# Optimization experiments

Measured on AMD Instinct MI355X. Metric: run time of the kernel, lower is better.

Reference implementation:

```python
import jax, jax.numpy as jnp
import numpy as np

IN_DIM = 64
OUT_DIM = 64
N_MODES = 32


def setup_inputs() -> dict:
    key = jax.random.key(0)
    k_x, k_w0, k_w1 = jax.random.split(key, 3)
    x = jax.random.normal(k_x, (32, IN_DIM, 128, 128), dtype=jnp.float32)
    # xavier_normal_ on tensor of shape (in, out, modes, 2): fan_in = out*modes*2, fan_out = in*modes*2? 
    # torch treats dim0 as fan_out-ish; exact init scale is irrelevant for correctness baselines,
    # so use a matching gaussian std = sqrt(2/(in_dim+out_dim)).
    std = float(np.sqrt(2.0 / (IN_DIM + OUT_DIM)))
    w0 = std * jax.random.normal(k_w0, (IN_DIM, OUT_DIM, N_MODES, 2), dtype=jnp.float32)
    w1 = std * jax.random.normal(k_w1, (IN_DIM, OUT_DIM, N_MODES, 2), dtype=jnp.float32)
    return {"x": x, "w0": w0, "w1": w1}


def reference(x, w0, w1):
    B, I, M, N = x.shape
    n_modes = w0.shape[2]

    # ---- width (last-axis) branch ----
    x_fty = jnp.fft.rfft(x, axis=-1, norm='ortho')                      # [B, I, M, N//2+1]
    wc0 = w0[..., 0] + 1j * w0[..., 1]                                  # [I, O, n_modes]
    low_y = jnp.einsum('bixy,ioy->boxy', x_fty[..., :n_modes], wc0)     # [B, O, M, n_modes]
    out_ft_y = jnp.pad(low_y, ((0, 0), (0, 0), (0, 0), (0, N // 2 + 1 - n_modes)))
    xy = jnp.fft.irfft(out_ft_y, n=N, axis=-1, norm='ortho')            # [B, O, M, N]

    # ---- height (second-to-last axis) branch ----
    x_ftx = jnp.fft.rfft(x, axis=-2, norm='ortho')                      # [B, I, M//2+1, N]
    wc1 = w1[..., 0] + 1j * w1[..., 1]                                  # [I, O, n_modes]
    low_x = jnp.einsum('bixy,iox->boxy', x_ftx[:, :, :n_modes, :], wc1)  # [B, O, n_modes, N]
    out_ft_x = jnp.pad(low_x, ((0, 0), (0, 0), (0, M // 2 + 1 - n_modes), (0, 0)))
    xx = jnp.fft.irfft(out_ft_x, n=M, axis=-2, norm='ortho')            # [B, O, M, N]

    return xx + xy
```

## Files before the change

### kernel.cpp

```cpp
#include <hip/hip_runtime.h>


typedef _Float16 half8  __attribute__((ext_vector_type(8)));
typedef _Float16 half4v __attribute__((ext_vector_type(4)));
typedef _Float16 half2v __attribute__((ext_vector_type(2)));
typedef float    floatx4 __attribute__((ext_vector_type(4)));

#define TWO_PI_OVER_128 0.049087385212340517f

__device__ __forceinline__ unsigned int packh2(float a, float b) {
    half2v h; h[0] = (_Float16)a; h[1] = (_Float16)b;
    return __builtin_bit_cast(unsigned int, h);
}
__device__ __forceinline__ half8  ash8(uint4 u) { return __builtin_bit_cast(half8, u); }
__device__ __forceinline__ half4v ash4(uint2 u) { return __builtin_bit_cast(half4v, u); }

#define MFMA_K16(A,B,C) __builtin_amdgcn_mfma_f32_16x16x16f16((A),(B),(C),0,0,0)

#define YS_PK 324
#define YS_PR 20

__global__ __launch_bounds__(256) void w2expand(const float* __restrict__ w0,
                                                const float* __restrict__ w1,
                                                uint2* __restrict__ W2h)
{
    int g = blockIdx.x * 256 + threadIdx.x;
    const float* w = (g >> 17) ? w1 : w0;
    int e    = g & 131071;
    int lane = e & 63;
    int m    = (e >> 6) & 7;
    int c    = (e >> 9) & 7;
    int k    = e >> 12;
    int mrow = lane & 15, q = lane >> 4;
    int o  = (m * 16 + mrow) >> 1;
    int oc = mrow & 1;
    unsigned int h2[2];
#pragma unroll
    for (int hp = 0; hp < 2; ++hp) {
        int i = c * 8 + q * 2 + hp;
        const float* wp = w + ((i * 64 + o) * 32 + k) * 2;
        float re = wp[0], im = wp[1];
        float v0 = oc ? im : re;
        float v1 = oc ? re : -im;
        h2[hp] = packh2(v0, v1);
    }
    W2h[g] = make_uint2(h2[0], h2[1]);
}

template<int BR>
__global__ __launch_bounds__(512, 4) void spectral(const float* __restrict__ x,
                                                   const uint2* __restrict__ w2,
                                                   float* __restrict__ out)
{
    __shared__ uint4 Ubuf[34816 / 16];
    __shared__ unsigned short Ys[32 * YS_PK];

    unsigned short* Xs = (unsigned short*)Ubuf;
    unsigned int*   Zs = (unsigned int*)Ubuf;

    const int tid  = threadIdx.x;
    const int wv   = tid >> 6;
    const int lane = tid & 63;
    const int mrow = tid & 15;
    const int quad = (tid >> 4) & 3;
    const int bx   = blockIdx.x;
    const int oh   = bx & 1;
    const int tile = (bx >> 1) & 7;
    const int b    = bx >> 4;

    const long xb = (long)b * 1048576 + (BR == 0 ? tile * 2048 : tile * 16);
    const long ob = xb;

    const int kptile = wv & 3;
    half8 Ff[4];
#pragma unroll
    for (int s = 0; s < 4; ++s)
#pragma unroll
        for (int j = 0; j < 8; ++j) {
            int d  = s * 32 + quad * 8 + j;
            int kp = kptile * 16 + mrow;
            int k  = kp >> 1;
            float ang = TWO_PI_OVER_128 * (float)((k * d) & 127);
            float v = (kp & 1) ? -sinf(ang) : cosf(ang);
            Ff[s][j] = (_Float16)v;
        }

    floatx4 acc[2][2][4];
#pragma unroll
    for (int a = 0; a < 2; ++a)
#pragma unroll
        for (int kk = 0; kk < 2; ++kk)
#pragma unroll
            for (int m = 0; m < 4; ++m)
                acc[a][kk][m] = (floatx4){0.f, 0.f, 0.f, 0.f};


#pragma unroll
    for (int g = 0; g < 2; ++g) {
        float4 v[4];
#pragma unroll
        for (int pp = 0; pp < 4; ++pp) {
            int p = g * 4 + pp;
            if (BR == 0) {
                int idx = p * 512 + tid;
                int col = idx >> 5, dg = idx & 31;
                v[pp] = *(const float4*)(x + xb + (long)(col >> 4) * 16384 + (col & 15) * 128 + dg * 4);
            } else {
                int d = (tid >> 2) & 127, tq = (tid & 3) * 4;
                v[pp] = *(const float4*)(x + xb + (long)p * 16384 + d * 128 + tq);
            }
        }
#pragma unroll
        for (int pp = 0; pp < 4; ++pp) {
            int p = g * 4 + pp;
            if (BR == 0) {
                int idx = p * 512 + tid;
                int col = idx >> 5, dg = idx & 31;
                *(uint2*)&Xs[col * 136 + dg * 4] =
                    make_uint2(packh2(v[pp].x, v[pp].y), packh2(v[pp].z, v[pp].w));
            } else {
                int d = (tid >> 2) & 127, tq = (tid & 3) * 4;
                int colb = p * 16 + tq;
                Xs[(colb + 0) * 136 + d] = __builtin_bit_cast(unsigned short, (_Float16)v[pp].x);
                Xs[(colb + 1) * 136 + d] = __builtin_bit_cast(unsigned short, (_Float16)v[pp].y);
                Xs[(colb + 2) * 136 + d] = __builtin_bit_cast(unsigned short, (_Float16)v[pp].z);
                Xs[(colb + 3) * 136 + d] = __builtin_bit_cast(unsigned short, (_Float16)v[pp].w);
            }
        }
    }
    __syncthreads();

    for (int c = 0; c < 8; ++c) {
        float4 pfA[4];
        if (c < 7) {
#pragma unroll
            for (int p = 0; p < 4; ++p) {
                if (BR == 0) {
                    int idx = p * 512 + tid;
                    int col = idx >> 5, dg = idx & 31;
                    pfA[p] = *(const float4*)(x + xb + (long)((c + 1) * 8 + (col >> 4)) * 16384 + (col & 15) * 128 + dg * 4);
                } else {
                    int d = (tid >> 2) & 127, tq = (tid & 3) * 4;
                    pfA[p] = *(const float4*)(x + xb + (long)((c + 1) * 8 + p) * 16384 + d * 128 + tq);
                }
            }
        }

#pragma unroll
        for (int cc = 0; cc < 4; ++cc) {
            int i = (wv >> 2) * 4 + cc;
            floatx4 y4 = {0.f, 0.f, 0.f, 0.f};
#pragma unroll
            for (int s = 0; s < 4; ++s) {
                uint4 bv = *(const uint4*)&Xs[(i * 16 + mrow) * 136 + s * 32 + quad * 8];
                y4 = __builtin_amdgcn_mfma_f32_16x16x32_f16(Ff[s], ash8(bv), y4, 0, 0, 0);
            }
            int k0 = kptile * 8 + quad * 2;
            unsigned int* yw = (unsigned int*)Ys;
            yw[(k0    ) * (YS_PK / 2) + mrow * (YS_PR / 2) + i] = packh2(y4[0], y4[1]);
            yw[(k0 + 1) * (YS_PK / 2) + mrow * (YS_PR / 2) + i] = packh2(y4[2], y4[3]);
        }
        __syncthreads();

        float4 pfB[4];
        if (c < 7) {
#pragma unroll
            for (int p = 0; p < 4; ++p) {
                if (BR == 0) {
                    int idx = p * 512 + tid;
                    int col = idx >> 5, dg = idx & 31;
                    *(uint2*)&Xs[col * 136 + dg * 4] =
                        make_uint2(packh2(pfA[p].x, pfA[p].y), packh2(pfA[p].z, pfA[p].w));
                } else {
                    int d = (tid >> 2) & 127, tq = (tid & 3) * 4;
                    int colb = p * 16 + tq;
                    Xs[(colb + 0) * 136 + d] = __builtin_bit_cast(unsigned short, (_Float16)pfA[p].x);
                    Xs[(colb + 1) * 136 + d] = __builtin_bit_cast(unsigned short, (_Float16)pfA[p].y);
                    Xs[(colb + 2) * 136 + d] = __builtin_bit_cast(unsigned short, (_Float16)pfA[p].z);
                    Xs[(colb + 3) * 136 + d] = __builtin_bit_cast(unsigned short, (_Float16)pfA[p].w);
                }
            }
#pragma unroll
            for (int p = 0; p < 4; ++p) {
                if (BR == 0) {
                    int idx = (p + 4) * 512 + tid;
                    int col = idx >> 5, dg = idx & 31;
                    pfB[p] = *(const float4*)(x + xb + (long)((c + 1) * 8 + (col >> 4)) * 16384 + (col & 15) * 128 + dg * 4);
                } else {
                    int d = (tid >> 2) & 127, tq = (tid & 3) * 4;
                    pfB[p] = *(const float4*)(x + xb + (long)((c + 1) * 8 + 4 + p) * 16384 + d * 128 + tq);
                }
            }
        }

        {
            half4v bfA0 = ash4(*(const uint2*)&Ys[(2 * wv     ) * YS_PK + mrow * YS_PR + quad * 4]);
            half4v bfA1 = ash4(*(const uint2*)&Ys[(2 * wv + 1 ) * YS_PK + mrow * YS_PR + quad * 4]);
            half4v bfB0 = ash4(*(const uint2*)&Ys[(2 * wv + 16) * YS_PK + mrow * YS_PR + quad * 4]);
            half4v bfB1 = ash4(*(const uint2*)&Ys[(2 * wv + 17) * YS_PK + mrow * YS_PR + quad * 4]);
            const uint2* wpA = w2 + (((2 * wv) * 8 + c) * 8 + oh * 4) * 64 + lane;
            const uint2* wpB = wpA + 65536;
#pragma unroll
            for (int m = 0; m < 4; ++m) {
                acc[0][0][m] = MFMA_K16(ash4(wpA[m * 64       ]), bfA0, acc[0][0][m]);
                acc[0][1][m] = MFMA_K16(ash4(wpA[m * 64 + 4096]), bfA1, acc[0][1][m]);
                acc[1][0][m] = MFMA_K16(ash4(wpB[m * 64       ]), bfB0, acc[1][0][m]);
                acc[1][1][m] = MFMA_K16(ash4(wpB[m * 64 + 4096]), bfB1, acc[1][1][m]);
            }
        }

        if (c < 7) {
#pragma unroll
            for (int p = 0; p < 4; ++p) {
                if (BR == 0) {
                    int idx = (p + 4) * 512 + tid;
                    int col = idx >> 5, dg = idx & 31;
                    *(uint2*)&Xs[col * 136 + dg * 4] =
                        make_uint2(packh2(pfB[p].x, pfB[p].y), packh2(pfB[p].z, pfB[p].w));
                } else {
                    int d = (tid >> 2) & 127, tq = (tid & 3) * 4;
                    int colb = (4 + p) * 16 + tq;
                    Xs[(colb + 0) * 136 + d] = __builtin_bit_cast(unsigned short, (_Float16)pfB[p].x);
                    Xs[(colb + 1) * 136 + d] = __builtin_bit_cast(unsigned short, (_Float16)pfB[p].y);
                    Xs[(colb + 2) * 136 + d] = __builtin_bit_cast(unsigned short, (_Float16)pfB[p].z);
                    Xs[(colb + 3) * 136 + d] = __builtin_bit_cast(unsigned short, (_Float16)pfB[p].w);
                }
            }
        }
        __syncthreads();
    }

    const int dt = wv;
    const int dp = dt * 16 + mrow;
    half8 Gf[2];
#pragma unroll
    for (int s = 0; s < 2; ++s)
#pragma unroll
        for (int j = 0; j < 8; ++j) {
            int kp = s * 32 + quad * 8 + j;
            int k  = kp >> 1;
            float ang = TWO_PI_OVER_128 * (float)((k * dp) & 127);
            float v;
            if (kp == 0)      v = 1.f / 128.f;
            else if (kp == 1) v = 0.f;
            else v = (kp & 1) ? -(2.f / 128.f) * sinf(ang) : (2.f / 128.f) * cosf(ang);
            Gf[s][j] = (_Float16)v;
        }

#pragma unroll
    for (int q = 0; q < 4; ++q) {
        __syncthreads();
#pragma unroll
        for (int a = 0; a < 2; ++a)
#pragma unroll
            for (int kk = 0; kk < 2; ++kk) {
                const int kmode = 2 * (wv + a * 8) + kk;
                const int slot  = kmode ^ (quad * 8);
                const int col   = (quad * 2) * 16 + mrow;
                Zs[ col       * 36 + slot] = packh2(acc[a][kk][q][0], acc[a][kk][q][1]);
                Zs[(col + 16) * 36 + slot] = packh2(acc[a][kk][q][2], acc[a][kk][q][3]);
            }
        __syncthreads();

#pragma unroll
        for (int cc = 0; cc < 8; ++cc) {
            const int ct  = cc;
            const int col = ct * 16 + mrow;
            const int swz = (ct & 6) << 2;
            floatx4 o4 = {0.f, 0.f, 0.f, 0.f};
#pragma unroll
            for (int s = 0; s < 2; ++s) {
                uint4 zv = *(const uint4*)&Zs[col * 36 + ((s * 16 + quad * 4) ^ swz)];
                o4 = __builtin_amdgcn_mfma_f32_16x16x32_f16(Gf[s], ash8(zv), o4, 0, 0, 0);
            }
            const int oo = oh * 32 + q * 8 + ct;
            const int t  = mrow;
            const int db = dt * 16 + quad * 4;
            if (BR == 0) {
                __builtin_nontemporal_store(o4, (floatx4*)(out + ob + (long)oo * 16384 + t * 128 + db));
            } else {
                float* p = out + ob + (long)oo * 16384 + (long)db * 128 + t;
                unsafeAtomicAdd(p,       o4[0]);
                unsafeAtomicAdd(p + 128, o4[1]);
                unsafeAtomicAdd(p + 256, o4[2]);
                unsafeAtomicAdd(p + 384, o4[3]);
            }
        }
    }
}

extern "C" void kernel_launch(void* const* d_in, const int* in_sizes, int n_in,
                              void* d_out, int out_size, void* d_ws, size_t ws_size,
                              hipStream_t stream) {
    const float* x  = (const float*)d_in[0];
    const float* w0 = (const float*)d_in[1];
    const float* w1 = (const float*)d_in[2];
    float* out = (float*)d_out;

    uint2* W2h = (uint2*)d_ws;

    w2expand<<<dim3(1024), dim3(256), 0, stream>>>(w0, w1, W2h);

    dim3 grid(512);
    dim3 block(512);

    spectral<0><<<grid, block, 0, stream>>>(x, W2h,          out);
    spectral<1><<<grid, block, 0, stream>>>(x, W2h + 131072, out);
}
```

Measured before the change: 574.5 us.

## Merge output-channel halves into one 1024-thread block with K32 MFMA mixing

Each block now covers all 64 output channels for its tile with 1024 threads, instead of two blocks each handling half the outputs and both redoing the forward DFT of the same input tile. The channel-mixing step switches from 16x16x16 to 16x16x32 MFMAs over 16 input channels per chunk, and the weight-expansion kernel writes a matching uint4 layout. This removes the duplicated input loads and forward DFT work. In exchange the grid drops to 256 blocks, and each block uses twice the shared memory and carries larger accumulator register tiles, which may lower occupancy.

```diff
diff --git a/kernel.cpp b/kernel.cpp
--- a/kernel.cpp
+++ b/kernel.cpp
@@ -2,7 +2,6 @@
 
 
 typedef _Float16 half8  __attribute__((ext_vector_type(8)));
-typedef _Float16 half4v __attribute__((ext_vector_type(4)));
 typedef _Float16 half2v __attribute__((ext_vector_type(2)));
 typedef float    floatx4 __attribute__((ext_vector_type(4)));
 
@@ -12,47 +11,51 @@
     half2v h; h[0] = (_Float16)a; h[1] = (_Float16)b;
     return __builtin_bit_cast(unsigned int, h);
 }
-__device__ __forceinline__ half8  ash8(uint4 u) { return __builtin_bit_cast(half8, u); }
-__device__ __forceinline__ half4v ash4(uint2 u) { return __builtin_bit_cast(half4v, u); }
-
-#define MFMA_K16(A,B,C) __builtin_amdgcn_mfma_f32_16x16x16f16((A),(B),(C),0,0,0)
-
-#define YS_PK 324
-#define YS_PR 20
+__device__ __forceinline__ half8 ash8(uint4 u) { return __builtin_bit_cast(half8, u); }
+
+#define MFMA_K32(A,B,C) __builtin_amdgcn_mfma_f32_16x16x32_f16((A),(B),(C),0,0,0)
+
+#define YS_PR 40
+#define YS_PK 648
 
 __global__ __launch_bounds__(256) void w2expand(const float* __restrict__ w0,
                                                 const float* __restrict__ w1,
-                                                uint2* __restrict__ W2h)
+                                                uint4* __restrict__ W2h)
 {
     int g = blockIdx.x * 256 + threadIdx.x;
-    const float* w = (g >> 17) ? w1 : w0;
-    int e    = g & 131071;
+    const float* w = (g >> 16) ? w1 : w0;
+    int e    = g & 65535;
     int lane = e & 63;
     int m    = (e >> 6) & 7;
-    int c    = (e >> 9) & 7;
-    int k    = e >> 12;
-    int mrow = lane & 15, q = lane >> 4;
+    int c4   = (e >> 9) & 3;
+    int k    = e >> 11;
+    int mrow = lane & 15, quad = lane >> 4;
     int o  = (m * 16 + mrow) >> 1;
     int oc = mrow & 1;
-    unsigned int h2[2];
-#pragma unroll
-    for (int hp = 0; hp < 2; ++hp) {
-        int i = c * 8 + q * 2 + hp;
-        const float* wp = w + ((i * 64 + o) * 32 + k) * 2;
-        float re = wp[0], im = wp[1];
-        float v0 = oc ? im : re;
-        float v1 = oc ? re : -im;
-        h2[hp] = packh2(v0, v1);
+    unsigned int hw[4];
+#pragma unroll
+    for (int jp = 0; jp < 4; ++jp) {
+        float v[2];
+#pragma unroll
+        for (int jj = 0; jj < 2; ++jj) {
+            int r    = quad * 8 + jp * 2 + jj;
+            int i    = c4 * 16 + (r >> 1);
+            int comp = r & 1;
+            const float* wp = w + ((i * 64 + o) * 32 + k) * 2;
+            float re = wp[0], im = wp[1];
+            v[jj] = oc ? (comp ? re : im) : (comp ? -im : re);
+        }
+        hw[jp] = packh2(v[0], v[1]);
     }
-    W2h[g] = make_uint2(h2[0], h2[1]);
+    W2h[g] = make_uint4(hw[0], hw[1], hw[2], hw[3]);
 }
 
 template<int BR>
-__global__ __launch_bounds__(512, 4) void spectral(const float* __restrict__ x,
-                                                   const uint2* __restrict__ w2,
-                                                   float* __restrict__ out)
+__global__ __launch_bounds__(1024, 4) void spectral(const float* __restrict__ x,
+                                                    const uint4* __restrict__ w2,
+                                                    float* __restrict__ out)
 {
-    __shared__ uint4 Ubuf[34816 / 16];
+    __shared__ uint4 Ubuf[69632 / 16];
     __shared__ unsigned short Ys[32 * YS_PK];
 
     unsigned short* Xs = (unsigned short*)Ubuf;
@@ -64,14 +67,14 @@
     const int mrow = tid & 15;
     const int quad = (tid >> 4) & 3;
     const int bx   = blockIdx.x;
-    const int oh   = bx & 1;
-    const int tile = (bx >> 1) & 7;
-    const int b    = bx >> 4;
+    const int b    = bx >> 3;
+    const int tile = bx & 7;
 
     const long xb = (long)b * 1048576 + (BR == 0 ? tile * 2048 : tile * 16);
     const long ob = xb;
 
     const int kptile = wv & 3;
+    const int igrp   = wv >> 2;
     half8 Ff[4];
 #pragma unroll
     for (int s = 0; s < 4; ++s)
@@ -85,15 +88,12 @@
             Ff[s][j] = (_Float16)v;
         }
 
-    floatx4 acc[2][2][4];
-#pragma unroll
-    for (int a = 0; a < 2; ++a)
-#pragma unroll
-        for (int kk = 0; kk < 2; ++kk)
-#pragma unroll
-            for (int m = 0; m < 4; ++m)
-                acc[a][kk][m] = (floatx4){0.f, 0.f, 0.f, 0.f};
-
+    floatx4 acc[2][8];
+#pragma unroll
+    for (int kk = 0; kk < 2; ++kk)
+#pragma unroll
+        for (int m = 0; m < 8; ++m)
+            acc[kk][m] = (floatx4){0.f, 0.f, 0.f, 0.f};
 
 #pragma unroll
     for (int g = 0; g < 2; ++g) {
@@ -102,25 +102,27 @@
         for (int pp = 0; pp < 4; ++pp) {
             int p = g * 4 + pp;
             if (BR == 0) {
-                int idx = p * 512 + tid;
+                int idx = p * 1024 + tid;
                 int col = idx >> 5, dg = idx & 31;
                 v[pp] = *(const float4*)(x + xb + (long)(col >> 4) * 16384 + (col & 15) * 128 + dg * 4);
             } else {
+                int i = (tid >> 9) + p * 2;
                 int d = (tid >> 2) & 127, tq = (tid & 3) * 4;
-                v[pp] = *(const float4*)(x + xb + (long)p * 16384 + d * 128 + tq);
+                v[pp] = *(const float4*)(x + xb + (long)i * 16384 + d * 128 + tq);
             }
         }
 #pragma unroll
         for (int pp = 0; pp < 4; ++pp) {
             int p = g * 4 + pp;
             if (BR == 0) {
-                int idx = p * 512 + tid;
+                int idx = p * 1024 + tid;
                 int col = idx >> 5, dg = idx & 31;
                 *(uint2*)&Xs[col * 136 + dg * 4] =
                     make_uint2(packh2(v[pp].x, v[pp].y), packh2(v[pp].z, v[pp].w));
             } else {
+                int i = (tid >> 9) + p * 2;
                 int d = (tid >> 2) & 127, tq = (tid & 3) * 4;
-                int colb = p * 16 + tq;
+                int colb = i * 16 + tq;
                 Xs[(colb + 0) * 136 + d] = __builtin_bit_cast(unsigned short, (_Float16)v[pp].x);
                 Xs[(colb + 1) * 136 + d] = __builtin_bit_cast(unsigned short, (_Float16)v[pp].y);
                 Xs[(colb + 2) * 136 + d] = __builtin_bit_cast(unsigned short, (_Float16)v[pp].z);
@@ -130,25 +132,26 @@
     }
     __syncthreads();
 
-    for (int c = 0; c < 8; ++c) {
+    for (int c = 0; c < 4; ++c) {
         float4 pfA[4];
-        if (c < 7) {
+        if (c < 3) {
 #pragma unroll
             for (int p = 0; p < 4; ++p) {
                 if (BR == 0) {
-                    int idx = p * 512 + tid;
+                    int idx = p * 1024 + tid;
                     int col = idx >> 5, dg = idx & 31;
-                    pfA[p] = *(const float4*)(x + xb + (long)((c + 1) * 8 + (col >> 4)) * 16384 + (col & 15) * 128 + dg * 4);
+                    pfA[p] = *(const float4*)(x + xb + (long)((c + 1) * 16 + (col >> 4)) * 16384 + (col & 15) * 128 + dg * 4);
                 } else {
+                    int i = (tid >> 9) + p * 2;
                     int d = (tid >> 2) & 127, tq = (tid & 3) * 4;
-                    pfA[p] = *(const float4*)(x + xb + (long)((c + 1) * 8 + p) * 16384 + d * 128 + tq);
+                    pfA[p] = *(const float4*)(x + xb + (long)((c + 1) * 16 + i) * 16384 + d * 128 + tq);
                 }
             }
         }
 
 #pragma unroll
         for (int cc = 0; cc < 4; ++cc) {
-            int i = (wv >> 2) * 4 + cc;
+            int i = igrp * 4 + cc;
             floatx4 y4 = {0.f, 0.f, 0.f, 0.f};
 #pragma unroll
             for (int s = 0; s < 4; ++s) {
@@ -163,17 +166,18 @@
         __syncthreads();
 
         float4 pfB[4];
-        if (c < 7) {
+        if (c < 3) {
 #pragma unroll
             for (int p = 0; p < 4; ++p) {
                 if (BR == 0) {
-                    int idx = p * 512 + tid;
+                    int idx = p * 1024 + tid;
                     int col = idx >> 5, dg = idx & 31;
                     *(uint2*)&Xs[col * 136 + dg * 4] =
                         make_uint2(packh2(pfA[p].x, pfA[p].y), packh2(pfA[p].z, pfA[p].w));
                 } else {
+                    int i = (tid >> 9) + p * 2;
                     int d = (tid >> 2) & 127, tq = (tid & 3) * 4;
-                    int colb = p * 16 + tq;
+                    int colb = i * 16 + tq;
                     Xs[(colb + 0) * 136 + d] = __builtin_bit_cast(unsigned short, (_Float16)pfA[p].x);
                     Xs[(colb + 1) * 136 + d] = __builtin_bit_cast(unsigned short, (_Float16)pfA[p].y);
                     Xs[(colb + 2) * 136 + d] = __builtin_bit_cast(unsigned short, (_Float16)pfA[p].z);
@@ -183,43 +187,40 @@
 #pragma unroll
             for (int p = 0; p < 4; ++p) {
                 if (BR == 0) {
-                    int idx = (p + 4) * 512 + tid;
+                    int idx = (p + 4) * 1024 + tid;
                     int col = idx >> 5, dg = idx & 31;
-                    pfB[p] = *(const float4*)(x + xb + (long)((c + 1) * 8 + (col >> 4)) * 16384 + (col & 15) * 128 + dg * 4);
+                    pfB[p] = *(const float4*)(x + xb + (long)((c + 1) * 16 + (col >> 4)) * 16384 + (col & 15) * 128 + dg * 4);
                 } else {
+                    int i = (tid >> 9) + (p + 4) * 2;
                     int d = (tid >> 2) & 127, tq = (tid & 3) * 4;
-                    pfB[p] = *(const float4*)(x + xb + (long)((c + 1) * 8 + 4 + p) * 16384 + d * 128 + tq);
+                    pfB[p] = *(const float4*)(x + xb + (long)((c + 1) * 16 + i) * 16384 + d * 128 + tq);
                 }
             }
         }
 
         {
-            half4v bfA0 = ash4(*(const uint2*)&Ys[(2 * wv     ) * YS_PK + mrow * YS_PR + quad * 4]);
-            half4v bfA1 = ash4(*(const uint2*)&Ys[(2 * wv + 1 ) * YS_PK + mrow * YS_PR + quad * 4]);
-            half4v bfB0 = ash4(*(const uint2*)&Ys[(2 * wv + 16) * YS_PK + mrow * YS_PR + quad * 4]);
-            half4v bfB1 = ash4(*(const uint2*)&Ys[(2 * wv + 17) * YS_PK + mrow * YS_PR + quad * 4]);
-            const uint2* wpA = w2 + (((2 * wv) * 8 + c) * 8 + oh * 4) * 64 + lane;
-            const uint2* wpB = wpA + 65536;
-#pragma unroll
-            for (int m = 0; m < 4; ++m) {
-                acc[0][0][m] = MFMA_K16(ash4(wpA[m * 64       ]), bfA0, acc[0][0][m]);
-                acc[0][1][m] = MFMA_K16(ash4(wpA[m * 64 + 4096]), bfA1, acc[0][1][m]);
-                acc[1][0][m] = MFMA_K16(ash4(wpB[m * 64       ]), bfB0, acc[1][0][m]);
-                acc[1][1][m] = MFMA_K16(ash4(wpB[m * 64 + 4096]), bfB1, acc[1][1][m]);
-            }
-        }
-
-        if (c < 7) {
+            half8 bf0 = ash8(*(const uint4*)&Ys[(2 * wv    ) * YS_PK + mrow * YS_PR + quad * 8]);
+            half8 bf1 = ash8(*(const uint4*)&Ys[(2 * wv + 1) * YS_PK + mrow * YS_PR + quad * 8]);
+            const uint4* wp = w2 + (((2 * wv) * 4 + c) * 8) * 64 + lane;
+#pragma unroll
+            for (int m = 0; m < 8; ++m) {
+                acc[0][m] = MFMA_K32(ash8(wp[m * 64       ]), bf0, acc[0][m]);
+                acc[1][m] = MFMA_K32(ash8(wp[m * 64 + 2048]), bf1, acc[1][m]);
+            }
+        }
+
+        if (c < 3) {
 #pragma unroll
             for (int p = 0; p < 4; ++p) {
                 if (BR == 0) {
-                    int idx = (p + 4) * 512 + tid;
+                    int idx = (p + 4) * 1024 + tid;
                     int col = idx >> 5, dg = idx & 31;
                     *(uint2*)&Xs[col * 136 + dg * 4] =
                         make_uint2(packh2(pfB[p].x, pfB[p].y), packh2(pfB[p].z, pfB[p].w));
                 } else {
+                    int i = (tid >> 9) + (p + 4) * 2;
                     int d = (tid >> 2) & 127, tq = (tid & 3) * 4;
-                    int colb = (4 + p) * 16 + tq;
+                    int colb = i * 16 + tq;
                     Xs[(colb + 0) * 136 + d] = __builtin_bit_cast(unsigned short, (_Float16)pfB[p].x);
                     Xs[(colb + 1) * 136 + d] = __builtin_bit_cast(unsigned short, (_Float16)pfB[p].y);
                     Xs[(colb + 2) * 136 + d] = __builtin_bit_cast(unsigned short, (_Float16)pfB[p].z);
@@ -230,8 +231,9 @@
         __syncthreads();
     }
 
-    const int dt = wv;
-    const int dp = dt * 16 + mrow;
+    const int dt  = wv & 7;
+    const int ctb = (wv >> 3) * 8;
+    const int dp  = dt * 16 + mrow;
     half8 Gf[2];
 #pragma unroll
     for (int s = 0; s < 2; ++s)
@@ -247,24 +249,24 @@
             Gf[s][j] = (_Float16)v;
         }
 
-#pragma unroll
     for (int q = 0; q < 4; ++q) {
         __syncthreads();
 #pragma unroll
-        for (int a = 0; a < 2; ++a)
+        for (int mm = 0; mm < 2; ++mm) {
+            const int m = q * 2 + mm;
 #pragma unroll
             for (int kk = 0; kk < 2; ++kk) {
-                const int kmode = 2 * (wv + a * 8) + kk;
-                const int slot  = kmode ^ (quad * 8);
-                const int col   = (quad * 2) * 16 + mrow;
-                Zs[ col       * 36 + slot] = packh2(acc[a][kk][q][0], acc[a][kk][q][1]);
-                Zs[(col + 16) * 36 + slot] = packh2(acc[a][kk][q][2], acc[a][kk][q][3]);
-            }
+                const int slot = (wv * 2 + kk) ^ (quad * 8);
+                const int col  = (mm * 8 + quad * 2) * 16 + mrow;
+                Zs[ col       * 36 + slot] = packh2(acc[kk][m][0], acc[kk][m][1]);
+                Zs[(col + 16) * 36 + slot] = packh2(acc[kk][m][2], acc[kk][m][3]);
+            }
+        }
         __syncthreads();
 
 #pragma unroll
         for (int cc = 0; cc < 8; ++cc) {
-            const int ct  = cc;
+            const int ct  = ctb + cc;
             const int col = ct * 16 + mrow;
             const int swz = (ct & 6) << 2;
             floatx4 o4 = {0.f, 0.f, 0.f, 0.f};
@@ -273,7 +275,7 @@
                 uint4 zv = *(const uint4*)&Zs[col * 36 + ((s * 16 + quad * 4) ^ swz)];
                 o4 = __builtin_amdgcn_mfma_f32_16x16x32_f16(Gf[s], ash8(zv), o4, 0, 0, 0);
             }
-            const int oo = oh * 32 + q * 8 + ct;
+            const int oo = q * 16 + ct;
             const int t  = mrow;
             const int db = dt * 16 + quad * 4;
             if (BR == 0) {
@@ -297,13 +299,13 @@
     const float* w1 = (const float*)d_in[2];
     float* out = (float*)d_out;
 
-    uint2* W2h = (uint2*)d_ws;
-
-    w2expand<<<dim3(1024), dim3(256), 0, stream>>>(w0, w1, W2h);
-
-    dim3 grid(512);
-    dim3 block(512);
-
-    spectral<0><<<grid, block, 0, stream>>>(x, W2h,          out);
-    spectral<1><<<grid, block, 0, stream>>>(x, W2h + 131072, out);
+    uint4* W2h = (uint4*)d_ws;
+
+    w2expand<<<dim3(512), dim3(256), 0, stream>>>(w0, w1, W2h);
+
+    dim3 grid(256);
+    dim3 block(1024);
+
+    spectral<0><<<grid, block, 0, stream>>>(x, W2h,         out);
+    spectral<1><<<grid, block, 0, stream>>>(x, W2h + 65536, out);
 }
```

After: 503.2 us. -12.4%, faster.
